# Optimization experiments

Measured on AMD Instinct MI355X. Metric: run time of the kernel, lower is better.

Reference implementation:

```python
import jax, jax.numpy as jnp
import numpy as np

# Constants hardcoded in SpikingNN.__init__
T, DT = 50.0, 0.125
PREF, PMIN, PTH = 0.0, -1.0, 25.0
D, PSPIKE, TREF = 0.25, 4.0, 5.0
TIME = jnp.asarray(np.arange(0, T + DT, DT), dtype=jnp.float32)  # [401]


def setup_inputs() -> dict:
    key = jax.random.key(0)
    k1, k2 = jax.random.split(key)
    N, L = 131072, TIME.shape[0]  # 131072 traces x 401 timesteps
    S = jax.random.uniform(k1, (N, L), dtype=jnp.float32)
    Pn = jax.random.normal(k2, (N, L), dtype=jnp.float32)  # never read before write; shape only
    return {"Pn": Pn, "S": S}


def _forward(S):
    # S: [N, L]; sequential LIF scan over time, vectorized over N traces.
    t0 = TIME[0]
    P0 = S[:, 0] - D                       # i == 0 branch
    spike0 = P0 >= PTH
    P0 = jnp.where(spike0, P0 + PSPIKE, P0)
    t_rest0 = jnp.where(spike0, t0 + TREF, jnp.zeros_like(P0))  # self.t_rest starts at 0

    def step(carry, xs):
        P_prev, t_rest = carry
        s, t = xs
        # refractory: clamp to Pref; else integrate if above Pmin, else reset to 0
        P = jnp.where(t <= t_rest, PREF,
                      jnp.where(P_prev > PMIN, P_prev + s - D, 0.0))
        spike = P >= PTH
        P = jnp.where(spike, P + PSPIKE, P)        # spike overshoot marker
        t_rest = jnp.where(spike, t + TREF, t_rest)  # enter refractory period
        return (P, t_rest), P

    # scan over time axis: xs are ([L-1, N] currents, [L-1] times)
    (_, _), Ps = jax.lax.scan(step, (P0, t_rest0), (S[:, 1:].T, TIME[1:]))
    return jnp.concatenate([P0[:, None], Ps.T], axis=1)  # [N, L]


def reference(Pn, S):
    # Pn is overwritten in-place in the original before any element is read.
    return _forward(S)
```

## Files before the change

kernel.cpp:

```cpp
#include <hip/hip_runtime.h>


#define L_STEPS 401
#define NCHUNK  13
#define CHUNK   32
#define BLKT    256
#define SLICE   (64 * CHUNK)

typedef const __attribute__((address_space(1))) void* gas1_t;
typedef __attribute__((address_space(3))) void*       las3_t;

__global__ __launch_bounds__(BLKT) void snn_scan_kernel(
    const float* __restrict__ S, float* __restrict__ out)
{
    __shared__ float smem[4][2][SLICE];

    const int tid       = threadIdx.x;
    const int wave      = tid >> 6;
    const int lane      = tid & 63;
    const int traceBase = blockIdx.x * BLKT + wave * 64;

    float P = 0.0f, t_rest = -1.0f;

    auto stage = [&](int ccol, int b) {
        #pragma unroll
        for (int k = 0; k < 32; ++k) {
            const int s_  = k * 64 + lane;
            const int row = s_ >> 5;
            const int col = (s_ & 31) ^ (row & 31);
            int gc = ccol + col;
            if (gc > 400) gc = 400;
            const float* gp = S + (traceBase + row) * L_STEPS + gc;
            __builtin_amdgcn_global_load_lds(
                (gas1_t)gp, (las3_t)&smem[wave][b][k * 64], 4, 0, 0);
        }
    };

    stage(0, 0);
    asm volatile("s_waitcnt vmcnt(0)" ::: "memory");

    #pragma unroll 1
    for (int c = 0; c < NCHUNK; ++c) {
        const int c0 = c * CHUNK;
        const int b  = c & 1;

        if (c) asm volatile("s_waitcnt vmcnt(32)" ::: "memory");

        float sv[CHUNK];
        #pragma unroll
        for (int j = 0; j < CHUNK; ++j)
            sv[j] = smem[wave][b][lane * CHUNK + (j ^ (lane & 31))];
        asm volatile("" ::: "memory");

        if (c + 1 < NCHUNK) stage(c0 + CHUNK, (c + 1) & 1);
        asm volatile("" ::: "memory");

        #pragma unroll
        for (int j = 0; j < CHUNK; ++j) {
            const float t = (float)(c0 + j) * 0.125f;
            float p = (t <= t_rest)
                    ? 0.0f
                    : ((P > -1.0f) ? (P + sv[j]) - 0.25f : 0.0f);
            const bool spike = (p >= 25.0f);
            t_rest = spike ? t + 5.0f : t_rest;
            p      = spike ? p + 4.0f : p;
            sv[j]  = p;
            P      = p;
        }

        #pragma unroll
        for (int j = 0; j < CHUNK; ++j)
            smem[wave][b][lane * CHUNK + (j ^ (lane & 31))] = sv[j];
        asm volatile("" ::: "memory");

        #pragma unroll
        for (int k = 0; k < 32; ++k) {
            const int s_  = k * 64 + lane;
            const int row = s_ >> 5;
            const int col = (s_ & 31) ^ (row & 31);
            const int gc  = c0 + col;
            if (gc < L_STEPS)
                out[(traceBase + row) * L_STEPS + gc] = smem[wave][b][s_];
        }
        asm volatile("" ::: "memory");
    }
}

extern "C" void kernel_launch(void* const* d_in, const int* in_sizes, int n_in,
                              void* d_out, int out_size, void* d_ws, size_t ws_size,
                              hipStream_t stream)
{
    const float* S   = (const float*)d_in[1];
    float*       out = (float*)d_out;

    snn_scan_kernel<<<(131072 / BLKT), BLKT, 0, stream>>>(S, out);
}
```

Before: 510.9 us.

## Triple-buffer input staging, shrink blocks, and vectorize output stores

Moves from double to triple buffering of the LDS-staged input chunks, prefetching two chunks ahead and tuning the vmcnt waits so loads overlap more compute and stores. Output stores are rewritten so each lane writes 4 consecutive floats per row as one vector store instead of 32 scalar stores per lane. Block size drops to 128 threads to keep LDS per block small with the third buffer. The hand-counted vmcnt thresholds are fragile, and because rows are 401 floats long the vector stores are unaligned.

```diff
diff --git a/kernel.cpp b/kernel.cpp
--- a/kernel.cpp
+++ b/kernel.cpp
@@ -4,16 +4,18 @@
 #define L_STEPS 401
 #define NCHUNK  13
 #define CHUNK   32
-#define BLKT    256
+#define BLKT    128
+#define NWAVES  (BLKT / 64)
 #define SLICE   (64 * CHUNK)
 
 typedef const __attribute__((address_space(1))) void* gas1_t;
 typedef __attribute__((address_space(3))) void*       las3_t;
+typedef float f4v __attribute__((ext_vector_type(4), aligned(4)));
 
 __global__ __launch_bounds__(BLKT) void snn_scan_kernel(
     const float* __restrict__ S, float* __restrict__ out)
 {
-    __shared__ float smem[4][2][SLICE];
+    __shared__ float smem[NWAVES][3][SLICE];
 
     const int tid       = threadIdx.x;
     const int wave      = tid >> 6;
@@ -30,30 +32,29 @@
             const int col = (s_ & 31) ^ (row & 31);
             int gc = ccol + col;
             if (gc > 400) gc = 400;
-            const float* gp = S + (traceBase + row) * L_STEPS + gc;
+            const float* gp = S + (size_t)(traceBase + row) * L_STEPS + gc;
             __builtin_amdgcn_global_load_lds(
                 (gas1_t)gp, (las3_t)&smem[wave][b][k * 64], 4, 0, 0);
         }
     };
 
-    stage(0, 0);
-    asm volatile("s_waitcnt vmcnt(0)" ::: "memory");
+    stage(0,     0);
+    stage(CHUNK, 1);
 
     #pragma unroll 1
     for (int c = 0; c < NCHUNK; ++c) {
         const int c0 = c * CHUNK;
-        const int b  = c & 1;
+        const int b  = c % 3;
 
-        if (c) asm volatile("s_waitcnt vmcnt(32)" ::: "memory");
+        if (c == 0)              asm volatile("s_waitcnt vmcnt(32)" ::: "memory");
+        else if (c == 1)         asm volatile("s_waitcnt vmcnt(40)" ::: "memory");
+        else if (c < NCHUNK - 1) asm volatile("s_waitcnt vmcnt(48)" ::: "memory");
+        else                     asm volatile("s_waitcnt vmcnt(16)" ::: "memory");
 
         float sv[CHUNK];
         #pragma unroll
         for (int j = 0; j < CHUNK; ++j)
             sv[j] = smem[wave][b][lane * CHUNK + (j ^ (lane & 31))];
-        asm volatile("" ::: "memory");
-
-        if (c + 1 < NCHUNK) stage(c0 + CHUNK, (c + 1) & 1);
-        asm volatile("" ::: "memory");
 
         #pragma unroll
         for (int j = 0; j < CHUNK; ++j) {
@@ -71,16 +72,34 @@
         #pragma unroll
         for (int j = 0; j < CHUNK; ++j)
             smem[wave][b][lane * CHUNK + (j ^ (lane & 31))] = sv[j];
+
         asm volatile("" ::: "memory");
 
-        #pragma unroll
-        for (int k = 0; k < 32; ++k) {
-            const int s_  = k * 64 + lane;
-            const int row = s_ >> 5;
-            const int col = (s_ & 31) ^ (row & 31);
-            const int gc  = c0 + col;
-            if (gc < L_STEPS)
-                out[(traceBase + row) * L_STEPS + gc] = smem[wave][b][s_];
+        if (c + 2 < NCHUNK) stage(c0 + 2 * CHUNK, (c + 2) % 3);
+        asm volatile("" ::: "memory");
+
+        {
+            const int q  = lane & 7;
+            const int rb = lane >> 3;
+            #pragma unroll
+            for (int k = 0; k < 8; ++k) {
+                const int r  = 8 * k + rb;
+                const int rx = r & 31;
+                const float v0 = smem[wave][b][r * CHUNK + ((4 * q + 0) ^ rx)];
+                const float v1 = smem[wave][b][r * CHUNK + ((4 * q + 1) ^ rx)];
+                const float v2 = smem[wave][b][r * CHUNK + ((4 * q + 2) ^ rx)];
+                const float v3 = smem[wave][b][r * CHUNK + ((4 * q + 3) ^ rx)];
+                const int gc = c0 + 4 * q;
+                float* op = out + (size_t)(traceBase + r) * L_STEPS + gc;
+                if (gc + 3 <= 400) {
+                    f4v v = {v0, v1, v2, v3};
+                    *(f4v*)op = v;
+                } else if (gc <= 400) {
+                    op[0] = v0;
+                    if (gc + 1 <= 400) op[1] = v1;
+                    if (gc + 2 <= 400) op[2] = v2;
+                }
+            }
         }
         asm volatile("" ::: "memory");
     }
```

New measurement: 521.7 us. +2.1%, slower.
